# Performance work log

Hardware: AMD Instinct MI355X
Metric: run time of the kernel (lower is better)

## Reference

```python
import jax, jax.numpy as jnp
import numpy as np

EMBED_DIM = 1024
HEAD_SIZE = 256
B, T = 8, 2048


def setup_inputs() -> dict:
    key = jax.random.key(0)
    kx, kq, kk, kv = jax.random.split(key, 4)
    x = jax.random.normal(kx, (B, T, EMBED_DIM), dtype=jnp.float32)
    # torch Linear(E, H, bias=False): weight [H, E], y = x @ W.T; store as [E, H]
    s = 1.0 / np.sqrt(EMBED_DIM)
    Wq = jax.random.uniform(kq, (EMBED_DIM, HEAD_SIZE), jnp.float32, -s, s)
    Wk = jax.random.uniform(kk, (EMBED_DIM, HEAD_SIZE), jnp.float32, -s, s)
    Wv = jax.random.uniform(kv, (EMBED_DIM, HEAD_SIZE), jnp.float32, -s, s)
    return {"x": x, "Wq": Wq, "Wk": Wk, "Wv": Wv}


def reference(x, Wq, Wk, Wv):
    # x: [B, T, E]
    q = jnp.einsum("bte,eh->bth", x, Wq)
    k = jnp.einsum("bte,eh->bth", x, Wk)
    v = jnp.einsum("bte,eh->bth", x, Wv)
    scale = HEAD_SIZE ** -0.5
    scores = jnp.einsum("bth,bsh->bts", q, k) * scale  # [B, T, T]
    t = x.shape[1]
    causal = jnp.tril(jnp.ones((t, t), dtype=bool))
    scores = jnp.where(causal, scores, -jnp.inf)
    attn = jax.nn.softmax(scores, axis=-1)  # dropout p=0.0 -> identity
    return jnp.einsum("bts,bsh->bth", attn, v)
```

## Files before the change

kernel.cpp:

```cpp
#include <hip/hip_runtime.h>
#include <stdint.h>

#define EMBED 1024
#define HEAD  256
#define BATCH 8
#define SEQ   2048
#define NTOK  (BATCH*SEQ)

typedef __attribute__((ext_vector_type(8)))  short  s16x8;
typedef __attribute__((ext_vector_type(4)))  float  f32x4;
typedef __attribute__((ext_vector_type(16))) float  f32x16;
typedef __attribute__((ext_vector_type(4)))  unsigned short u16x4;

__device__ __forceinline__ unsigned short f2bf(float f) {
  union { float f; uint32_t u; } v; v.f = f;
  return (unsigned short)((v.u + 0x7FFFu + ((v.u >> 16) & 1u)) >> 16);
}

__device__ __forceinline__ uint32_t cvtpk(float a, float b) {
  uint32_t r;
  asm("v_cvt_pk_bf16_f32 %0, %1, %2" : "=v"(r) : "v"(a), "v"(b));
  return r;
}

__device__ __forceinline__ void gload_lds16(const void* g, void* l) {
  __builtin_amdgcn_global_load_lds((const __attribute__((address_space(1))) void*)g,
                                   (__attribute__((address_space(3))) void*)l, 16, 0, 0);
}

__global__ __launch_bounds__(256) void wt_kernel(const float* __restrict__ Wq,
                                                 const float* __restrict__ Wk,
                                                 const float* __restrict__ Wv,
                                                 unsigned short* __restrict__ Wt) {
  int idx = blockIdx.x * 256 + threadIdx.x;
  int e  = idx & (EMBED - 1);
  int hw = idx >> 10;
  int w  = hw >> 8;
  int h  = hw & 255;
  const float* W = (w == 0) ? Wq : (w == 1) ? Wk : Wv;
  float sc = (w == 0) ? 0.0625f : 1.0f;
  Wt[idx] = f2bf(W[(size_t)e * HEAD + h] * sc);
}

__global__ __launch_bounds__(256) void xprep_kernel(const float* __restrict__ x,
                                                    unsigned short* __restrict__ xb) {
  size_t i8 = ((size_t)blockIdx.x * 256 + threadIdx.x) * 8;
  f32x4 f0 = *(const f32x4*)(x + i8);
  f32x4 f1 = *(const f32x4*)(x + i8 + 4);
  u16x4 p0, p1;
  #pragma unroll
  for (int j = 0; j < 4; j++) { p0[j] = f2bf(f0[j]); p1[j] = f2bf(f1[j]); }
  *(u16x4*)(xb + i8)     = p0;
  *(u16x4*)(xb + i8 + 4) = p1;
}

__global__ __launch_bounds__(256) void proj_kernel(const unsigned short* __restrict__ xb,
    const unsigned short* __restrict__ Wt,
    unsigned short* __restrict__ qo, unsigned short* __restrict__ ko,
    unsigned short* __restrict__ vfrag) {
  __shared__ unsigned short Al[128 * 64];
  __shared__ unsigned short Bl[128 * 64];
  const int tid  = threadIdx.x;
  const int lane = tid & 63;
  const int wid  = tid >> 6;
  const int wm = wid >> 1, wn = wid & 1;
  const int bid  = blockIdx.x;
  const int xcd  = bid & 7;
  const int i6   = bid >> 3;
  const int mloc = i6 & 15;
  const int nz   = i6 >> 4;
  const int m0 = (xcd * 16 + mloc) * 128;
  const int n0 = (nz & 1) * 128;
  const int w  = nz >> 1;
  const unsigned short* Wtw = Wt + (size_t)w * 256 * EMBED;

  f32x4 acc[4][4] = {};

  for (int k0 = 0; k0 < EMBED; k0 += 64) {
    #pragma unroll
    for (int i = 0; i < 4; i++) {
      int u = tid + 256 * i;
      int row = u >> 3, sc = u & 7;
      gload_lds16(xb + (size_t)(m0 + row) * EMBED + k0 + sc * 8,
                  &Al[i * 2048 + wid * 512]);
    }
    #pragma unroll
    for (int i = 0; i < 4; i++) {
      int u = tid + 256 * i;
      int row = u >> 3, sc = u & 7;
      gload_lds16(Wtw + (size_t)(n0 + row) * EMBED + k0 + sc * 8,
                  &Bl[i * 2048 + wid * 512]);
    }
    __syncthreads();
    #pragma unroll
    for (int kk = 0; kk < 2; kk++) {
      s16x8 a[4], bfr[4];
      #pragma unroll
      for (int mi = 0; mi < 4; mi++) {
        int row = wm * 64 + mi * 16 + (lane & 15);
        a[mi] = *(const s16x8*)(&Al[row * 64 + kk * 32 + 8 * (lane >> 4)]);
      }
      #pragma unroll
      for (int ni = 0; ni < 4; ni++) {
        int row = wn * 64 + ni * 16 + (lane & 15);
        bfr[ni] = *(const s16x8*)(&Bl[row * 64 + kk * 32 + 8 * (lane >> 4)]);
      }
      #pragma unroll
      for (int mi = 0; mi < 4; mi++)
        #pragma unroll
        for (int ni = 0; ni < 4; ni++)
          acc[mi][ni] = __builtin_amdgcn_mfma_f32_16x16x32_bf16(a[mi], bfr[ni], acc[mi][ni], 0, 0, 0);
    }
    __syncthreads();
  }

  if (w < 2) {
    unsigned short* dst = (w == 0) ? qo : ko;
    #pragma unroll
    for (int mi = 0; mi < 4; mi++)
      #pragma unroll
      for (int r = 0; r < 4; r++) {
        int mrow = m0 + wm * 64 + mi * 16 + 4 * (lane >> 4) + r;
        #pragma unroll
        for (int ni = 0; ni < 4; ni++) {
          int col = n0 + wn * 64 + ni * 16 + (lane & 15);
          dst[(size_t)mrow * HEAD + col] = f2bf(acc[mi][ni][r]);
        }
      }
  } else {
    #pragma unroll
    for (int mi = 0; mi < 4; mi++) {
      int base = m0 + wm * 64 + mi * 16 + 4 * (lane >> 4);
      int toko = base & 31;
      size_t vb0 = (size_t)(base >> 11) * 524288
                 + (size_t)((base & 2047) >> 5) * 8192
                 + ((toko >> 4) & 1) * 512 + ((toko >> 3) & 1) * 256 + (toko & 7);
      #pragma unroll
      for (int ni = 0; ni < 4; ni++) {
        int col = n0 + wn * 64 + ni * 16 + (lane & 15);
        u16x4 pk;
        #pragma unroll
        for (int r = 0; r < 4; r++) pk[r] = f2bf(acc[mi][ni][r]);
        *(u16x4*)(vfrag + vb0 + (size_t)(col >> 5) * 1024 + (col & 31) * 8) = pk;
      }
    }
  }
}

__global__ __launch_bounds__(256, 1) void attn_kernel(const unsigned short* __restrict__ qb,
    const unsigned short* __restrict__ kb, const unsigned short* __restrict__ vfrag,
    float* __restrict__ out) {
  __shared__ unsigned short Kl[4][32 * 256];
  __shared__ float mls[4][2][32];
  const int tid  = threadIdx.x;
  const int lane = tid & 63;
  const int w    = tid >> 6;
  const int hi   = lane >> 5;
  const int q    = lane & 31;
  const int bid  = blockIdx.x;
  const int b = bid & 7;
  const int g = (bid >> 3) & 31;
  const int t = (bid < 256) ? (63 - g) : g;
  const unsigned short* qB = qb + (size_t)b * SEQ * HEAD;
  const unsigned short* kB = kb + (size_t)b * SEQ * HEAD;
  const unsigned short* vfB = vfrag + (size_t)b * 524288;
  float* outB = out + (size_t)b * SEQ * HEAD;
  const int qg = t * 32 + q;

  s16x8 qf[16];
  #pragma unroll
  for (int s = 0; s < 16; s++)
    qf[s] = *(const s16x8*)(qB + (size_t)qg * HEAD + s * 16 + hi * 8);

  f32x16 o[8] = {};
  float m = -1e30f, lsum = 0.f;

  const int nt = t + 1;
  const int cl = (nt + 3) >> 2;
  const int j0 = w * cl;
  const int j1 = (j0 + cl < nt) ? (j0 + cl) : nt;
  unsigned short* Kw = (unsigned short*)Kl[w];

  for (int j = j0; j < j1; j++) {
    #pragma unroll
    for (int i = 0; i < 16; i++) {
      int cl_ = i * 64 + lane;
      int key = cl_ >> 5, c = cl_ & 31;
      gload_lds16(kB + (size_t)(j * 32 + key) * HEAD + (size_t)((c ^ (key & 15)) * 8),
                  &Kw[i * 512]);
    }
    asm volatile("s_waitcnt vmcnt(0)" ::: "memory");
    __builtin_amdgcn_sched_barrier(0);
    f32x16 s0 = {}, s1 = {};
    #pragma unroll
    for (int s = 0; s < 8; s++) {
      s16x8 kf = *(const s16x8*)((const char*)Kw +
                   (q * 512 + (((2 * s + hi) ^ (q & 15)) << 4)));
      s0 = __builtin_amdgcn_mfma_f32_32x32x16_bf16(kf, qf[s], s0, 0, 0, 0);
    }
    #pragma unroll
    for (int s = 8; s < 16; s++) {
      s16x8 kf = *(const s16x8*)((const char*)Kw +
                   (q * 512 + (((2 * s + hi) ^ (q & 15)) << 4)));
      s1 = __builtin_amdgcn_mfma_f32_32x32x16_bf16(kf, qf[s], s1, 0, 0, 0);
    }
    f32x16 sv;
    #pragma unroll
    for (int r = 0; r < 16; r++) sv[r] = s0[r] + s1[r];
    if (j == t) {
      #pragma unroll
      for (int r = 0; r < 16; r++) {
        int kg = j * 32 + (r & 3) + 8 * (r >> 2) + 4 * hi;
        sv[r] = (kg > qg) ? -1e30f : sv[r];
      }
    }
    float mt = sv[0];
    #pragma unroll
    for (int r = 1; r < 16; r++) mt = fmaxf(mt, sv[r]);
    mt = fmaxf(mt, __shfl_xor(mt, 32));
    float mn = fmaxf(m, mt);
    if (!__all(mt - m <= 8.0f)) {
      float al = __expf(m - mn);
      lsum *= al;
      #pragma unroll
      for (int ht = 0; ht < 8; ht++)
        #pragma unroll
        for (int r = 0; r < 16; r++) o[ht][r] *= al;
      m = mn;
    }
    #pragma unroll
    for (int r = 0; r < 16; r++) sv[r] = __expf(sv[r] - m);
    float rs = 0.f;
    #pragma unroll
    for (int r = 0; r < 16; r++) rs += sv[r];
    rs += __shfl_xor(rs, 32);
    lsum += rs;
    uint32_t cc[8], dd[8];
    #pragma unroll
    for (int i = 0; i < 8; i++) cc[i] = cvtpk(sv[2 * i], sv[2 * i + 1]);
    #pragma unroll
    for (int i = 0; i < 8; i++) dd[i] = (uint32_t)__shfl_xor((int)cc[i], 32);
    union { s16x8 v; uint32_t u[4]; } pf0, pf1;
    pf0.u[0] = hi ? dd[2] : cc[0];
    pf0.u[1] = hi ? dd[3] : cc[1];
    pf0.u[2] = hi ? cc[2] : dd[0];
    pf0.u[3] = hi ? cc[3] : dd[1];
    pf1.u[0] = hi ? dd[6] : cc[4];
    pf1.u[1] = hi ? dd[7] : cc[5];
    pf1.u[2] = hi ? cc[6] : dd[4];
    pf1.u[3] = hi ? cc[7] : dd[5];
    const unsigned short* vT = vfB + (size_t)j * 8192 + hi * 256 + q * 8;
    #pragma unroll
    for (int ht = 0; ht < 8; ht++) {
      s16x8 vf0 = *(const s16x8*)(vT + ht * 1024);
      o[ht] = __builtin_amdgcn_mfma_f32_32x32x16_bf16(vf0, pf0.v, o[ht], 0, 0, 0);
      s16x8 vf1 = *(const s16x8*)(vT + ht * 1024 + 512);
      o[ht] = __builtin_amdgcn_mfma_f32_32x32x16_bf16(vf1, pf1.v, o[ht], 0, 0, 0);
    }
  }

  __syncthreads();
  if (lane < 32) { mls[w][0][q] = m; mls[w][1][q] = lsum; }
  __syncthreads();
  float mx = mls[0][0][q];
  #pragma unroll
  for (int w2 = 1; w2 < 4; w2++) mx = fmaxf(mx, mls[w2][0][q]);
  float L = 0.f;
  #pragma unroll
  for (int w2 = 0; w2 < 4; w2++)
    L += __expf(mls[w2][0][q] - mx) * mls[w2][1][q];
  float aown = __expf(m - mx);
  #pragma unroll
  for (int ht = 0; ht < 8; ht++)
    #pragma unroll
    for (int r = 0; r < 16; r++) o[ht][r] *= aown;

  float* obuf = (float*)&Kl[0][0];
  for (int ph = 3; ph >= 0; ph--) {
    if (w == ph) {
      #pragma unroll
      for (int ht = 0; ht < 8; ht++)
        #pragma unroll
        for (int g2 = 0; g2 < 4; g2++) {
          int gp = 8 * ht + 2 * g2 + hi;
          float* p = &obuf[q * 256 + ((gp ^ (q & 15)) << 2)];
          f32x4 v4 = { o[ht][4*g2], o[ht][4*g2+1], o[ht][4*g2+2], o[ht][4*g2+3] };
          if (ph != 3) { f32x4 prev = *(f32x4*)p;
            #pragma unroll
            for (int z = 0; z < 4; z++) v4[z] += prev[z]; }
          if (ph != 0) { *(f32x4*)p = v4; }
          else {
            #pragma unroll
            for (int z = 0; z < 4; z++) v4[z] /= L;
            *(f32x4*)(outB + (size_t)qg * HEAD + ht * 32 + g2 * 8 + hi * 4) = v4;
          }
        }
    }
    __syncthreads();
  }
}

extern "C" void kernel_launch(void* const* d_in, const int* in_sizes, int n_in,
                              void* d_out, int out_size, void* d_ws, size_t ws_size,
                              hipStream_t stream) {
  const float* x  = (const float*)d_in[0];
  const float* Wq = (const float*)d_in[1];
  const float* Wk = (const float*)d_in[2];
  const float* Wv = (const float*)d_in[3];
  float* out = (float*)d_out;

  unsigned short* ws = (unsigned short*)d_ws;
  unsigned short* qb    = ws;
  unsigned short* kb    = qb + (size_t)NTOK * HEAD;
  unsigned short* vfrag = kb + (size_t)NTOK * HEAD;
  unsigned short* Wt    = vfrag + (size_t)NTOK * HEAD;
  unsigned short* xb    = Wt + (size_t)3 * HEAD * EMBED;

  hipLaunchKernelGGL(wt_kernel, dim3(3 * 256 * EMBED / 256), dim3(256), 0, stream,
                     Wq, Wk, Wv, Wt);
  hipLaunchKernelGGL(xprep_kernel, dim3(NTOK * EMBED / (256 * 8)), dim3(256), 0, stream,
                     x, xb);
  hipLaunchKernelGGL(proj_kernel, dim3(768), dim3(256), 0, stream,
                     xb, Wt, qb, kb, vfrag);
  hipLaunchKernelGGL(attn_kernel, dim3(512), dim3(256), 0, stream,
                     qb, kb, vfrag, out);
}
```

Before: 149.7 us.

## Pair long and short causal query tiles in 8-wave attention blocks

The attention kernel now launches 256 blocks of 512 threads. Each block handles two query tiles of one batch: a long tile (63-p) and a short tile (p). The 8 waves are split between the two tiles in proportion to their key-tile counts, and partial softmax results are merged per group through LDS. The aim is to balance causal work per block and per CU instead of relying on the scheduler to pair heavy and light blocks. The launch bounds change to (512,2). That may cap VGPRs per wave sharply for a kernel that holds large accumulators and Q fragments in registers, so it risks spilling, and LDS use doubles to about 128KB.

```diff
diff --git a/kernel.cpp b/kernel.cpp
--- a/kernel.cpp
+++ b/kernel.cpp
@@ -147,11 +147,11 @@
   }
 }
 
-__global__ __launch_bounds__(256, 1) void attn_kernel(const unsigned short* __restrict__ qb,
+__global__ __launch_bounds__(512, 2) void attn_kernel(const unsigned short* __restrict__ qb,
     const unsigned short* __restrict__ kb, const unsigned short* __restrict__ vfrag,
     float* __restrict__ out) {
-  __shared__ unsigned short Kl[4][32 * 256];
-  __shared__ float mls[4][2][32];
+  __shared__ unsigned short Kl[8][32 * 256];
+  __shared__ float mls[8][2][32];
   const int tid  = threadIdx.x;
   const int lane = tid & 63;
   const int w    = tid >> 6;
@@ -159,8 +159,16 @@
   const int q    = lane & 31;
   const int bid  = blockIdx.x;
   const int b = bid & 7;
-  const int g = (bid >> 3) & 31;
-  const int t = (bid < 256) ? (63 - g) : g;
+  const int p = bid >> 3;
+  const int nta = 64 - p, ntb = p + 1;
+  int wa = (8 * nta + 32) / 65;
+  wa = (wa < 1) ? 1 : (wa > 7 ? 7 : wa);
+  const bool inA = (w < wa);
+  const int t    = inA ? (63 - p) : p;
+  const int nt   = inA ? nta : ntb;
+  const int gsz  = inA ? wa : (8 - wa);
+  const int base = inA ? 0 : wa;
+  const int rel  = w - base;
   const unsigned short* qB = qb + (size_t)b * SEQ * HEAD;
   const unsigned short* kB = kb + (size_t)b * SEQ * HEAD;
   const unsigned short* vfB = vfrag + (size_t)b * 524288;
@@ -175,9 +183,8 @@
   f32x16 o[8] = {};
   float m = -1e30f, lsum = 0.f;
 
-  const int nt = t + 1;
-  const int cl = (nt + 3) >> 2;
-  const int j0 = w * cl;
+  const int cl = (nt + gsz - 1) / gsz;
+  const int j0 = rel * cl;
   const int j1 = (j0 + cl < nt) ? (j0 + cl) : nt;
   unsigned short* Kw = (unsigned short*)Kl[w];
 
@@ -262,34 +269,40 @@
   __syncthreads();
   if (lane < 32) { mls[w][0][q] = m; mls[w][1][q] = lsum; }
   __syncthreads();
-  float mx = mls[0][0][q];
-  #pragma unroll
-  for (int w2 = 1; w2 < 4; w2++) mx = fmaxf(mx, mls[w2][0][q]);
+  float mx = mls[base][0][q];
+  for (int i = 1; i < gsz; i++) mx = fmaxf(mx, mls[base + i][0][q]);
   float L = 0.f;
-  #pragma unroll
-  for (int w2 = 0; w2 < 4; w2++)
-    L += __expf(mls[w2][0][q] - mx) * mls[w2][1][q];
+  for (int i = 0; i < gsz; i++)
+    L += __expf(mls[base + i][0][q] - mx) * mls[base + i][1][q];
   float aown = __expf(m - mx);
   #pragma unroll
   for (int ht = 0; ht < 8; ht++)
     #pragma unroll
     for (int r = 0; r < 16; r++) o[ht][r] *= aown;
 
-  float* obuf = (float*)&Kl[0][0];
-  for (int ph = 3; ph >= 0; ph--) {
-    if (w == ph) {
+  float* obufS = (float*)&Kl[inA ? 0 : 2][0];
+  for (int ph = 7; ph >= 0; ph--) {
+    if (rel == ph) {
       #pragma unroll
       for (int ht = 0; ht < 8; ht++)
         #pragma unroll
         for (int g2 = 0; g2 < 4; g2++) {
           int gp = 8 * ht + 2 * g2 + hi;
-          float* p = &obuf[q * 256 + ((gp ^ (q & 15)) << 2)];
+          float* ptr = &obufS[q * 256 + ((gp ^ (q & 15)) << 2)];
           f32x4 v4 = { o[ht][4*g2], o[ht][4*g2+1], o[ht][4*g2+2], o[ht][4*g2+3] };
-          if (ph != 3) { f32x4 prev = *(f32x4*)p;
+          if (ph == gsz - 1 && gsz > 1) {
+            *(f32x4*)ptr = v4;
+          } else if (ph > 0) {
+            f32x4 prev = *(f32x4*)ptr;
             #pragma unroll
-            for (int z = 0; z < 4; z++) v4[z] += prev[z]; }
-          if (ph != 0) { *(f32x4*)p = v4; }
-          else {
+            for (int z = 0; z < 4; z++) v4[z] += prev[z];
+            *(f32x4*)ptr = v4;
+          } else {
+            if (gsz > 1) {
+              f32x4 prev = *(f32x4*)ptr;
+              #pragma unroll
+              for (int z = 0; z < 4; z++) v4[z] += prev[z];
+            }
             #pragma unroll
             for (int z = 0; z < 4; z++) v4[z] /= L;
             *(f32x4*)(outB + (size_t)qg * HEAD + ht * 32 + g2 * 8 + hi * 4) = v4;
@@ -322,6 +335,6 @@
                      x, xb);
   hipLaunchKernelGGL(proj_kernel, dim3(768), dim3(256), 0, stream,
                      xb, Wt, qb, kb, vfrag);
-  hipLaunchKernelGGL(attn_kernel, dim3(512), dim3(256), 0, stream,
+  hipLaunchKernelGGL(attn_kernel, dim3(256), dim3(512), 0, stream,
                      qb, kb, vfrag, out);
 }
```

After: 186.2 us. +24.4%, slower.
